# Kernel tuning notes

Measured on AMD Instinct MI355X. Metric: run time of the kernel, lower is better.

Reference implementation:

```python
import jax, jax.numpy as jnp
from jax import lax
import numpy as np

B, CIN, COUT, H, W = 8, 3, 16, 384, 384
WSCALE = 0.15  # keeps initial mean|x| < 3 so the while loop runs a few iterations


def conv1x1(x, w, b):
    # x: [B,C,H,W], w: [O,C], b: [O] -- 1x1 conv == channel-mixing GEMM
    return jnp.einsum('bchw,oc->bohw', x, w) + b[None, :, None, None]


def setup_inputs() -> dict:
    key = jax.random.key(0)
    ks = jax.random.split(key, 4)
    x = jax.random.normal(ks[0], (B, CIN, H, W), dtype=jnp.float32)
    w_pre = jax.random.normal(ks[1], (COUT, CIN), dtype=jnp.float32) * WSCALE
    b_pre = jnp.zeros((COUT,), dtype=jnp.float32)
    w_loop = jax.random.normal(ks[2], (COUT, COUT), dtype=jnp.float32) * WSCALE
    b_loop = jnp.zeros((COUT,), dtype=jnp.float32)
    w_shared = jax.random.normal(ks[3], (COUT, COUT), dtype=jnp.float32) * WSCALE
    b_shared = jnp.zeros((COUT,), dtype=jnp.float32)
    return {"x": x, "w_pre": w_pre, "b_pre": b_pre, "w_loop": w_loop,
            "b_loop": b_loop, "w_shared": w_shared, "b_shared": b_shared}


def reference(x, w_pre, b_pre, w_loop, b_loop, w_shared, b_shared):
    x = conv1x1(x, w_pre, b_pre)

    def cond_fn(v):
        return jnp.mean(jnp.abs(v)) < 3.0

    def body_fn(v):
        v = conv1x1(v, w_shared, b_shared)
        v = jnp.tanh(v)
        v = conv1x1(v, w_loop, b_loop)
        return v * 10.0

    x = lax.while_loop(cond_fn, body_fn, x)
    return conv1x1(x, w_shared, b_shared)
```

## Files before the change

kernel.cpp:

```cpp
#include <hip/hip_runtime.h>
#include <math.h>

#define BQ   8
#define CIN  3
#define COUT 16
#define HW   (384 * 384)
#define NPIX (BQ * HW)
#define NELT ((double)NPIX * COUT)
#define MAX_ITERS 16

#define TPB       256
#define NBLK      512
#define NTHREADS  (NBLK * TPB)
#define PPT       9

typedef float vfloat16 __attribute__((ext_vector_type(16)));

struct Ctl {
    double sum[MAX_ITERS + 1];
    int    bar_count;
    int    bar_sense;
};

__global__ void k_init(Ctl* c) {
    int t = threadIdx.x;
    if (t <= MAX_ITERS) c->sum[t] = 0.0;
    if (t == 0) { c->bar_count = 0; c->bar_sense = 0; }
}

__device__ __forceinline__ float tanh_fast(float x) {
    float e = __expf(2.0f * x);
    return fmaf(-2.0f, __builtin_amdgcn_rcpf(e + 1.0f), 1.0f);
}

__device__ __forceinline__ float block_reduce_add(float v) {
    #pragma unroll
    for (int off = 32; off > 0; off >>= 1)
        v += __shfl_down(v, off, 64);
    __shared__ float red[TPB / 64];
    int lane = threadIdx.x & 63;
    int wid  = threadIdx.x >> 6;
    if (lane == 0) red[wid] = v;
    __syncthreads();
    float r = 0.f;
    if (threadIdx.x == 0) {
        #pragma unroll
        for (int i = 0; i < TPB / 64; ++i) r += red[i];
    }
    return r;
}

__device__ __forceinline__ void grid_barrier(Ctl* c, int* sense_sh) {
    __syncthreads();
    if (threadIdx.x == 0) {
        int next = *sense_sh ^ 1;
        int prev = __hip_atomic_fetch_add(&c->bar_count, 1, __ATOMIC_ACQ_REL,
                                          __HIP_MEMORY_SCOPE_AGENT);
        if (prev == NBLK - 1) {
            __hip_atomic_store(&c->bar_count, 0, __ATOMIC_RELAXED,
                               __HIP_MEMORY_SCOPE_AGENT);
            __hip_atomic_store(&c->bar_sense, next, __ATOMIC_RELEASE,
                               __HIP_MEMORY_SCOPE_AGENT);
        } else {
            while (__hip_atomic_load(&c->bar_sense, __ATOMIC_ACQUIRE,
                                     __HIP_MEMORY_SCOPE_AGENT) != next)
                __builtin_amdgcn_s_sleep(8);
        }
        *sense_sh = next;
    }
    __syncthreads();
}


#define PRE_PIXEL(vk, kk)                                                \
    { int p = tid + (kk) * NTHREADS; int b = p / HW; int hw = p - b * HW;\
      const float* xb = x + (size_t)b * (CIN * HW) + hw;                 \
      float x0 = xb[0], x1 = xb[HW], x2 = xb[2 * HW];                    \
      _Pragma("unroll")                                                  \
      for (int o = 0; o < COUT; ++o) {                                   \
          float a = bp[o];                                               \
          a = fmaf(wp[o * CIN + 0], x0, a);                              \
          a = fmaf(wp[o * CIN + 1], x1, a);                              \
          a = fmaf(wp[o * CIN + 2], x2, a);                              \
          vk[o] = a; s += fabsf(a);                                      \
      } }

#define STEP_PIXEL(vk)                                                   \
    { float tt[COUT];                                                    \
      _Pragma("unroll")                                                  \
      for (int o = 0; o < COUT; ++o) {                                   \
          float a = bs[o];                                               \
          _Pragma("unroll")                                              \
          for (int c = 0; c < COUT; ++c)                                 \
              a = fmaf(ws[o * COUT + c], vk[c], a);                      \
          tt[o] = tanh_fast(a);                                          \
      }                                                                  \
      _Pragma("unroll")                                                  \
      for (int o = 0; o < COUT; ++o) {                                   \
          float a = bl[o];                                               \
          _Pragma("unroll")                                              \
          for (int c = 0; c < COUT; ++c)                                 \
              a = fmaf(wl[o * COUT + c], tt[c], a);                      \
          a *= 10.f;                                                     \
          vk[o] = a; s += fabsf(a);                                      \
      } }

#define FIN_PIXEL(vk, kk)                                                \
    { int p = tid + (kk) * NTHREADS; int b = p / HW; int hw = p - b * HW;\
      float* ob = out + (size_t)b * (COUT * HW) + hw;                    \
      _Pragma("unroll")                                                  \
      for (int o = 0; o < COUT; ++o) {                                   \
          float a = bs[o];                                               \
          _Pragma("unroll")                                              \
          for (int c = 0; c < COUT; ++c)                                 \
              a = fmaf(ws[o * COUT + c], vk[c], a);                      \
          ob[(size_t)o * HW] = a;                                        \
      } }

__global__ __launch_bounds__(TPB, 2) void k_persist(
        const float* __restrict__ x,
        const float* __restrict__ wp, const float* __restrict__ bp,
        const float* __restrict__ wl, const float* __restrict__ bl,
        const float* __restrict__ ws, const float* __restrict__ bs,
        float* __restrict__ out, Ctl* __restrict__ ctl) {
    __shared__ int sense_sh;
    const int t = threadIdx.x;
    if (t == 0) sense_sh = 0;
    __syncthreads();

    const int tid = blockIdx.x * TPB + t;

    vfloat16 v0, v1, v2, v3, v4, v5, v6, v7, v8;

    float s = 0.f;
    PRE_PIXEL(v0, 0) PRE_PIXEL(v1, 1) PRE_PIXEL(v2, 2)
    PRE_PIXEL(v3, 3) PRE_PIXEL(v4, 4) PRE_PIXEL(v5, 5)
    PRE_PIXEL(v6, 6) PRE_PIXEL(v7, 7) PRE_PIXEL(v8, 8)
    {
        float r = block_reduce_add(s);
        if (t == 0) atomicAdd(&ctl->sum[0], (double)r);
    }
    grid_barrier(ctl, &sense_sh);

    int it = 0;
    while (it < MAX_ITERS) {
        double sv = __hip_atomic_load(&ctl->sum[it], __ATOMIC_ACQUIRE,
                                      __HIP_MEMORY_SCOPE_AGENT);
        if (sv / NELT >= 3.0) break;

        s = 0.f;
        STEP_PIXEL(v0) STEP_PIXEL(v1) STEP_PIXEL(v2)
        STEP_PIXEL(v3) STEP_PIXEL(v4) STEP_PIXEL(v5)
        STEP_PIXEL(v6) STEP_PIXEL(v7) STEP_PIXEL(v8)
        ++it;
        float r = block_reduce_add(s);
        if (t == 0) atomicAdd(&ctl->sum[it], (double)r);
        grid_barrier(ctl, &sense_sh);
    }

    FIN_PIXEL(v0, 0) FIN_PIXEL(v1, 1) FIN_PIXEL(v2, 2)
    FIN_PIXEL(v3, 3) FIN_PIXEL(v4, 4) FIN_PIXEL(v5, 5)
    FIN_PIXEL(v6, 6) FIN_PIXEL(v7, 7) FIN_PIXEL(v8, 8)
}

extern "C" void kernel_launch(void* const* d_in, const int* in_sizes, int n_in,
                              void* d_out, int out_size, void* d_ws, size_t ws_size,
                              hipStream_t stream) {
    const float* x  = (const float*)d_in[0];
    const float* wp = (const float*)d_in[1];
    const float* bp = (const float*)d_in[2];
    const float* wl = (const float*)d_in[3];
    const float* bl = (const float*)d_in[4];
    const float* ws = (const float*)d_in[5];
    const float* bs = (const float*)d_in[6];
    float* out = (float*)d_out;
    Ctl*   ctl = (Ctl*)d_ws;

    k_init<<<1, 64, 0, stream>>>(ctl);
    k_persist<<<NBLK, TPB, 0, stream>>>(x, wp, bp, wl, bl, ws, bs, out, ctl);
}
```

Baseline: 476.5 us.

## Use hierarchical grid barrier and per-block partial sums instead of contended atomics

Replaces the single-counter grid barrier with a two-level tree of padded leaf counters and a root counter, so fewer blocks contend on one cache line. Drops the double-precision atomicAdd of the abs-sum in favour of each block storing its float partial into its own slot, which every block then reads and reduces in one wavefront. This aims to cut atomic contention and serialization at each iteration's synchronisation point. In exchange every block re-reads all 512 partials each iteration, and the threshold test now uses a float sum in a different order, which could flip the loop decision near the boundary.

```diff
diff --git a/kernel.cpp b/kernel.cpp
--- a/kernel.cpp
+++ b/kernel.cpp
@@ -6,7 +6,7 @@
 #define COUT 16
 #define HW   (384 * 384)
 #define NPIX (BQ * HW)
-#define NELT ((double)NPIX * COUT)
+#define NELT 18874368.0f
 #define MAX_ITERS 16
 
 #define TPB       256
@@ -14,18 +14,24 @@
 #define NTHREADS  (NBLK * TPB)
 #define PPT       9
 
+#define NLEAF        64
+#define BLK_PER_LEAF (NBLK / NLEAF)
+
 typedef float vfloat16 __attribute__((ext_vector_type(16)));
 
+struct __align__(64) PadCnt { int cnt; int pad[15]; };
+
 struct Ctl {
-    double sum[MAX_ITERS + 1];
-    int    bar_count;
-    int    bar_sense;
+    PadCnt leaf[NLEAF];
+    PadCnt root;
+    PadCnt sense;
+    float  partials[MAX_ITERS + 1][NBLK];
 };
 
 __global__ void k_init(Ctl* c) {
     int t = threadIdx.x;
-    if (t <= MAX_ITERS) c->sum[t] = 0.0;
-    if (t == 0) { c->bar_count = 0; c->bar_sense = 0; }
+    if (t < NLEAF) c->leaf[t].cnt = 0;
+    if (t == 0) { c->root.cnt = 0; c->sense.cnt = 0; }
 }
 
 __device__ __forceinline__ float tanh_fast(float x) {
@@ -54,21 +60,44 @@
     __syncthreads();
     if (threadIdx.x == 0) {
         int next = *sense_sh ^ 1;
-        int prev = __hip_atomic_fetch_add(&c->bar_count, 1, __ATOMIC_ACQ_REL,
-                                          __HIP_MEMORY_SCOPE_AGENT);
-        if (prev == NBLK - 1) {
-            __hip_atomic_store(&c->bar_count, 0, __ATOMIC_RELAXED,
+        int lf = blockIdx.x & (NLEAF - 1);
+        int p = __hip_atomic_fetch_add(&c->leaf[lf].cnt, 1, __ATOMIC_ACQ_REL,
+                                       __HIP_MEMORY_SCOPE_AGENT);
+        if (p == BLK_PER_LEAF - 1) {
+            __hip_atomic_store(&c->leaf[lf].cnt, 0, __ATOMIC_RELAXED,
                                __HIP_MEMORY_SCOPE_AGENT);
-            __hip_atomic_store(&c->bar_sense, next, __ATOMIC_RELEASE,
-                               __HIP_MEMORY_SCOPE_AGENT);
-        } else {
-            while (__hip_atomic_load(&c->bar_sense, __ATOMIC_ACQUIRE,
-                                     __HIP_MEMORY_SCOPE_AGENT) != next)
-                __builtin_amdgcn_s_sleep(8);
+            int q = __hip_atomic_fetch_add(&c->root.cnt, 1, __ATOMIC_ACQ_REL,
+                                           __HIP_MEMORY_SCOPE_AGENT);
+            if (q == NLEAF - 1) {
+                __hip_atomic_store(&c->root.cnt, 0, __ATOMIC_RELAXED,
+                                   __HIP_MEMORY_SCOPE_AGENT);
+                __hip_atomic_store(&c->sense.cnt, next, __ATOMIC_RELEASE,
+                                   __HIP_MEMORY_SCOPE_AGENT);
+            }
         }
+        while (__hip_atomic_load(&c->sense.cnt, __ATOMIC_ACQUIRE,
+                                 __HIP_MEMORY_SCOPE_AGENT) != next)
+            __builtin_amdgcn_s_sleep(4);
         *sense_sh = next;
     }
     __syncthreads();
+}
+
+__device__ __forceinline__ float grid_sum(const float* part, float* bc) {
+    int lane = threadIdx.x & 63, wid = threadIdx.x >> 6;
+    if (wid == 0) {
+        float s = 0.f;
+        #pragma unroll
+        for (int i = 0; i < NBLK / 64; ++i)
+            s += __hip_atomic_load(&part[i * 64 + lane], __ATOMIC_RELAXED,
+                                   __HIP_MEMORY_SCOPE_AGENT);
+        #pragma unroll
+        for (int off = 32; off > 0; off >>= 1)
+            s += __shfl_down(s, off, 64);
+        if (lane == 0) *bc = s;
+    }
+    __syncthreads();
+    return *bc;
 }
 
 
@@ -124,6 +153,7 @@
         const float* __restrict__ ws, const float* __restrict__ bs,
         float* __restrict__ out, Ctl* __restrict__ ctl) {
     __shared__ int sense_sh;
+    __shared__ float bcast;
     const int t = threadIdx.x;
     if (t == 0) sense_sh = 0;
     __syncthreads();
@@ -138,15 +168,16 @@
     PRE_PIXEL(v6, 6) PRE_PIXEL(v7, 7) PRE_PIXEL(v8, 8)
     {
         float r = block_reduce_add(s);
-        if (t == 0) atomicAdd(&ctl->sum[0], (double)r);
+        if (t == 0)
+            __hip_atomic_store(&ctl->partials[0][blockIdx.x], r,
+                               __ATOMIC_RELAXED, __HIP_MEMORY_SCOPE_AGENT);
     }
     grid_barrier(ctl, &sense_sh);
 
     int it = 0;
     while (it < MAX_ITERS) {
-        double sv = __hip_atomic_load(&ctl->sum[it], __ATOMIC_ACQUIRE,
-                                      __HIP_MEMORY_SCOPE_AGENT);
-        if (sv / NELT >= 3.0) break;
+        float total = grid_sum(ctl->partials[it], &bcast);
+        if (total >= 3.0f * NELT) break;
 
         s = 0.f;
         STEP_PIXEL(v0) STEP_PIXEL(v1) STEP_PIXEL(v2)
@@ -154,7 +185,9 @@
         STEP_PIXEL(v6) STEP_PIXEL(v7) STEP_PIXEL(v8)
         ++it;
         float r = block_reduce_add(s);
-        if (t == 0) atomicAdd(&ctl->sum[it], (double)r);
+        if (t == 0)
+            __hip_atomic_store(&ctl->partials[it][blockIdx.x], r,
+                               __ATOMIC_RELAXED, __HIP_MEMORY_SCOPE_AGENT);
         grid_barrier(ctl, &sense_sh);
     }
 
```

After: 443.5 us. 6.9% less time.
